# Performance work log

Measured on AMD Instinct MI355X. Metric: run time of the kernel, lower is better.

Reference implementation:

```python
import jax, jax.numpy as jnp
import numpy as np

N = 50000      # nodes
E = 800000     # edges (before self-loops)
IN = 256       # in_channels
HID = 128      # hidden_channels
OUT = 128      # out_channels
NEG_SLOPE = 0.2
EPS = 1e-16


def setup_inputs() -> dict:
    key = jax.random.key(0)
    ks = jax.random.split(key, 16)
    p = lambda k, shape: jax.random.normal(k, shape, jnp.float32) * 0.1
    return {
        "x": jax.random.normal(ks[0], (N, IN), jnp.float32),
        "edge_index": jax.random.randint(ks[1], (2, E), 0, N, dtype=jnp.int64),
        # semantic MLP
        "W1": p(ks[2], (IN, HID)), "b1": jnp.zeros((HID,), jnp.float32),
        "W2": p(ks[3], (HID, HID)), "b2": jnp.zeros((HID,), jnp.float32),
        # gat1: HID -> HID//2, heads=4, concat -> 2*HID
        "g1_W": p(ks[4], (HID, 4 * (HID // 2))),
        "g1_as": p(ks[5], (4, HID // 2)), "g1_ad": p(ks[6], (4, HID // 2)),
        "g1_b": jnp.zeros((4 * (HID // 2),), jnp.float32),
        # gat2: 2*HID -> OUT, heads=2, mean -> OUT
        "g2_W": p(ks[7], (2 * HID, 2 * OUT)),
        "g2_as": p(ks[8], (2, OUT)), "g2_ad": p(ks[9], (2, OUT)),
        "g2_b": jnp.zeros((OUT,), jnp.float32),
        # gat3: OUT -> OUT, heads=1, mean -> OUT
        "g3_W": p(ks[10], (OUT, OUT)),
        "g3_as": p(ks[11], (1, OUT)), "g3_ad": p(ks[12], (1, OUT)),
        "g3_b": jnp.zeros((OUT,), jnp.float32),
    }


def _gat(h_in, src, dst, W, a_src, a_dst, bias, heads, concat, n):
    # Linear projection into heads: [n, H, C]
    h = (h_in @ W).reshape(n, heads, -1)
    alpha_s = jnp.sum(h * a_src[None], axis=-1)  # [n, H]
    alpha_d = jnp.sum(h * a_dst[None], axis=-1)  # [n, H]
    e = jax.nn.leaky_relu(alpha_s[src] + alpha_d[dst], NEG_SLOPE)  # [E', H]
    # segment softmax over edges grouped by destination node
    m = jax.ops.segment_max(e, dst, num_segments=n)
    ex = jnp.exp(e - m[dst])
    denom = jax.ops.segment_sum(ex, dst, num_segments=n)
    alpha = ex / (denom[dst] + EPS)  # [E', H]
    msg = h[src] * alpha[..., None]  # [E', H, C]
    out = jax.ops.segment_sum(msg, dst, num_segments=n)  # [n, H, C]
    out = out.reshape(n, -1) if concat else out.mean(axis=1)
    return out + bias


def reference(x, edge_index, W1, b1, W2, b2,
              g1_W, g1_as, g1_ad, g1_b,
              g2_W, g2_as, g2_ad, g2_b,
              g3_W, g3_as, g3_ad, g3_b):
    n = x.shape[0]
    # PyG GATConv add_self_loops=True: append self-loop edges once
    loops = jnp.arange(n, dtype=edge_index.dtype)
    src = jnp.concatenate([edge_index[0], loops])
    dst = jnp.concatenate([edge_index[1], loops])
    # semantic MLP (inference: dropout = identity)
    h = jax.nn.relu(x @ W1 + b1)
    h = jax.nn.relu(h @ W2 + b2)
    h = jax.nn.elu(_gat(h, src, dst, g1_W, g1_as, g1_ad, g1_b, 4, True, n))
    h = jax.nn.elu(_gat(h, src, dst, g2_W, g2_as, g2_ad, g2_b, 2, False, n))
    h = _gat(h, src, dst, g3_W, g3_as, g3_ad, g3_b, 1, False, n)
    return h
```

## Files before the change

kernel.cpp:

```cpp
#include <hip/hip_runtime.h>
#include <math.h>


#define NEG_SLOPE 0.2f
#define EPS_DEN 1e-16f

typedef __attribute__((ext_vector_type(8))) short short8;
typedef __attribute__((ext_vector_type(4))) float f32x4;
typedef __attribute__((ext_vector_type(2))) float f32x2;
typedef __attribute__((ext_vector_type(4))) unsigned short u16x4;

__device__ inline unsigned short f2b(float f) {
  unsigned u = __builtin_bit_cast(unsigned, f);
  unsigned r = (u + 0x7fffu + ((u >> 16) & 1u)) >> 16;
  return (unsigned short)r;
}
__device__ inline float b2f(unsigned short u) {
  return __builtin_bit_cast(float, (unsigned)u << 16);
}

__device__ inline void glds16(const void* g, void* l) {
  __builtin_amdgcn_global_load_lds(
      (const __attribute__((address_space(1))) void*)g,
      (__attribute__((address_space(3))) void*)l, 16, 0, 0);
}

__device__ inline f32x2 pk_fma(f32x2 a, f32x2 b, f32x2 c) {
  f32x2 d;
  asm("v_pk_fma_f32 %0, %1, %2, %3" : "=v"(d) : "v"(a), "v"(b), "v"(c));
  return d;
}

__device__ inline void accum8(f32x2 acc2[4], const short8 r, float w) {
  const f32x2 wv = {w, w};
  const unsigned* u = (const unsigned*)&r;
#pragma unroll
  for (int p = 0; p < 4; p++) {
    const unsigned lo = u[p] << 16;
    const unsigned hi = u[p] & 0xffff0000u;
    f32x2 val = {__builtin_bit_cast(float, lo), __builtin_bit_cast(float, hi)};
    acc2[p] = pk_fma(val, wv, acc2[p]);
  }
}

template <int H>
__device__ inline void loadH(const float* p, float* v) {
  if constexpr (H == 4) {
    float4 t = *(const float4*)p;
    v[0] = t.x; v[1] = t.y; v[2] = t.z; v[3] = t.w;
  } else if constexpr (H == 2) {
    float2 t = *(const float2*)p;
    v[0] = t.x; v[1] = t.y;
  } else {
    v[0] = *p;
  }
}

template <int ACT, int OBF, int H, int CC>
__global__ __launch_bounds__(256) void mfma_gemm(
    const unsigned short* __restrict__ A, const unsigned short* __restrict__ Bt,
    const float* __restrict__ bias, float* __restrict__ Cf,
    unsigned short* __restrict__ Cb, const float* __restrict__ a_s,
    const float* __restrict__ a_d, float* __restrict__ alS,
    float* __restrict__ alD, int n, int K, int M) {
  __shared__ unsigned short As[128 * 64];
  __shared__ unsigned short Bs[128 * 64];

  const int tid = threadIdx.x;
  const int w = tid >> 6, lane = tid & 63;
  const int row0 = blockIdx.x * 128, col0 = blockIdx.y * 128;
  const int lr = lane >> 3, lg = lane & 7;
  const int lm = lane & 15, kg = lane >> 4;
  const int wm = (w >> 1) * 64, wn = (w & 1) * 64;

  f32x4 acc[4][4];
#pragma unroll
  for (int i = 0; i < 4; i++)
#pragma unroll
    for (int j = 0; j < 4; j++) acc[i][j] = {0.f, 0.f, 0.f, 0.f};

  const int swz = (lg ^ lr) << 3;

  for (int k0 = 0; k0 < K; k0 += 64) {
    __syncthreads();
#pragma unroll
    for (int it = 0; it < 4; it++) {
      const int r = w * 32 + it * 8;
      glds16(A + (size_t)(row0 + r + lr) * K + k0 + swz, &As[r * 64]);
      glds16(Bt + (size_t)(col0 + r + lr) * K + k0 + swz, &Bs[r * 64]);
    }
    __syncthreads();

#pragma unroll
    for (int kh = 0; kh < 2; kh++) {
      const int sw = ((kh * 4 + kg) ^ (lm & 7)) << 3;
      short8 aF[4], bF[4];
#pragma unroll
      for (int i = 0; i < 4; i++) {
        aF[i] = *(const short8*)&As[(wm + i * 16 + lm) * 64 + sw];
        bF[i] = *(const short8*)&Bs[(wn + i * 16 + lm) * 64 + sw];
      }
#pragma unroll
      for (int i = 0; i < 4; i++)
#pragma unroll
        for (int j = 0; j < 4; j++)
          acc[i][j] = __builtin_amdgcn_mfma_f32_16x16x32_bf16(
              aF[i], bF[j], acc[i][j], 0, 0, 0);
    }
  }

  const int r4 = kg * 4;

  if constexpr (H > 0) {
    const int head = (col0 + wn) / CC;
    const int ch0 = (col0 + wn) % CC;
    float asv[4], adv[4];
#pragma unroll
    for (int j = 0; j < 4; j++) {
      asv[j] = a_s[head * CC + ch0 + j * 16 + lm];
      adv[j] = a_d[head * CC + ch0 + j * 16 + lm];
    }
#pragma unroll
    for (int i = 0; i < 4; i++) {
#pragma unroll
      for (int r = 0; r < 4; r++) {
        float ps = 0.f, pd = 0.f;
#pragma unroll
        for (int j = 0; j < 4; j++) {
          ps += acc[i][j][r] * asv[j];
          pd += acc[i][j][r] * adv[j];
        }
#pragma unroll
        for (int off = 1; off < 16; off <<= 1) {
          ps += __shfl_xor(ps, off, 64);
          pd += __shfl_xor(pd, off, 64);
        }
        if (lm == 0) {
          const int row = row0 + wm + i * 16 + r4 + r;
          if (row < n) {
            atomicAdd(&alS[(size_t)row * H + head], ps);
            atomicAdd(&alD[(size_t)row * H + head], pd);
          }
        }
      }
    }
  }

#pragma unroll
  for (int j = 0; j < 4; j++) {
    const int col = col0 + wn + j * 16 + lm;
    const float bv = bias ? bias[col] : 0.f;
#pragma unroll
    for (int i = 0; i < 4; i++) {
#pragma unroll
      for (int r = 0; r < 4; r++) {
        const int row = row0 + wm + i * 16 + r4 + r;
        if (row < n) {
          float v = acc[i][j][r] + bv;
          if (ACT == 1) v = v > 0.f ? v : 0.f;
          if (OBF)
            Cb[(size_t)row * M + col] = f2b(v);
          else
            Cf[(size_t)row * M + col] = v;
        }
      }
    }
  }
}

__global__ __launch_bounds__(256) void mlp_fused_kernel(
    const unsigned short* __restrict__ X, const unsigned short* __restrict__ W1t,
    const float* __restrict__ b1, const unsigned short* __restrict__ W2t,
    const float* __restrict__ b2, unsigned short* __restrict__ H2, int n) {
  __shared__ unsigned short As[128 * 64];
  __shared__ unsigned short Bs[128 * 64];
  __shared__ unsigned short H1s[128 * 136];

  const int tid = threadIdx.x;
  const int w = tid >> 6, lane = tid & 63;
  const int row0 = blockIdx.x * 128;
  const int lr = lane >> 3, lg = lane & 7;
  const int lm = lane & 15, kg = lane >> 4;
  const int wm = (w >> 1) * 64, wn = (w & 1) * 64;
  const int swz = (lg ^ lr) << 3;
  const int r4 = kg * 4;

  f32x4 acc[4][4];
#pragma unroll
  for (int i = 0; i < 4; i++)
#pragma unroll
    for (int j = 0; j < 4; j++) acc[i][j] = {0.f, 0.f, 0.f, 0.f};

  for (int k0 = 0; k0 < 256; k0 += 64) {
    __syncthreads();
#pragma unroll
    for (int it = 0; it < 4; it++) {
      const int r = w * 32 + it * 8;
      glds16(X + (size_t)(row0 + r + lr) * 256 + k0 + swz, &As[r * 64]);
      glds16(W1t + (size_t)(r + lr) * 256 + k0 + swz, &Bs[r * 64]);
    }
    __syncthreads();
#pragma unroll
    for (int kh = 0; kh < 2; kh++) {
      const int sw = ((kh * 4 + kg) ^ (lm & 7)) << 3;
      short8 aF[4], bF[4];
#pragma unroll
      for (int i = 0; i < 4; i++) {
        aF[i] = *(const short8*)&As[(wm + i * 16 + lm) * 64 + sw];
        bF[i] = *(const short8*)&Bs[(wn + i * 16 + lm) * 64 + sw];
      }
#pragma unroll
      for (int i = 0; i < 4; i++)
#pragma unroll
        for (int j = 0; j < 4; j++)
          acc[i][j] = __builtin_amdgcn_mfma_f32_16x16x32_bf16(
              aF[i], bF[j], acc[i][j], 0, 0, 0);
    }
  }

#pragma unroll
  for (int j = 0; j < 4; j++) {
    const int col = wn + j * 16 + lm;
    const float bv = b1[col];
#pragma unroll
    for (int i = 0; i < 4; i++) {
#pragma unroll
      for (int r = 0; r < 4; r++) {
        const int lrow = wm + i * 16 + r4 + r;
        float v = acc[i][j][r] + bv;
        v = v > 0.f ? v : 0.f;
        H1s[lrow * 136 + col] = f2b(v);
      }
    }
  }
#pragma unroll
  for (int i = 0; i < 4; i++)
#pragma unroll
    for (int j = 0; j < 4; j++) acc[i][j] = {0.f, 0.f, 0.f, 0.f};
  __syncthreads();

  for (int k0 = 0; k0 < 128; k0 += 64) {
    __syncthreads();
#pragma unroll
    for (int it = 0; it < 4; it++) {
      const int r = w * 32 + it * 8;
      glds16(W2t + (size_t)(r + lr) * 128 + k0 + swz, &Bs[r * 64]);
    }
    __syncthreads();
#pragma unroll
    for (int kh = 0; kh < 2; kh++) {
      const int swB = ((kh * 4 + kg) ^ (lm & 7)) << 3;
      const int kofs = k0 + (kh * 4 + kg) * 8;
      short8 aF[4], bF[4];
#pragma unroll
      for (int i = 0; i < 4; i++) {
        aF[i] = *(const short8*)&H1s[(wm + i * 16 + lm) * 136 + kofs];
        bF[i] = *(const short8*)&Bs[(wn + i * 16 + lm) * 64 + swB];
      }
#pragma unroll
      for (int i = 0; i < 4; i++)
#pragma unroll
        for (int j = 0; j < 4; j++)
          acc[i][j] = __builtin_amdgcn_mfma_f32_16x16x32_bf16(
              aF[i], bF[j], acc[i][j], 0, 0, 0);
    }
  }

#pragma unroll
  for (int j = 0; j < 4; j++) {
    const int col = wn + j * 16 + lm;
    const float bv = b2[col];
#pragma unroll
    for (int i = 0; i < 4; i++) {
#pragma unroll
      for (int r = 0; r < 4; r++) {
        const int row = row0 + wm + i * 16 + r4 + r;
        if (row < n) {
          float v = acc[i][j][r] + bv;
          v = v > 0.f ? v : 0.f;
          H2[(size_t)row * 128 + col] = f2b(v);
        }
      }
    }
  }
}

struct PrepArgs {
  const float* x; unsigned short* xb; long long nx;
  const float* W[5]; unsigned short* Wt[5];
  int K[5], M[5], t0[6];
  int* deg; int N;
  float* alz; long long nz;
};

__global__ __launch_bounds__(256) void fused_prep_kernel(PrepArgs a) {
  const int tid = threadIdx.x, bid = blockIdx.x, nb = gridDim.x;
  const long long gt = (long long)bid * 256 + tid;
  const long long gsz = (long long)nb * 256;
  __shared__ float tt[32][33];

  for (long long i = gt; i < a.N; i += gsz) a.deg[i] = 0;
  for (long long i = gt * 4; i < a.nz; i += gsz * 4)
    *(float4*)(a.alz + i) = make_float4(0.f, 0.f, 0.f, 0.f);
  for (long long i = gt * 4; i < a.nx; i += gsz * 4) {
    float4 v = *(const float4*)(a.x + i);
    u16x4 u = {f2b(v.x), f2b(v.y), f2b(v.z), f2b(v.w)};
    *(u16x4*)(a.xb + i) = u;
  }
  for (int t = bid; t < a.t0[5]; t += nb) {
    int di = 0;
    while (t >= a.t0[di + 1]) di++;
    const int local = t - a.t0[di];
    const int K = a.K[di], M = a.M[di], mtiles = M / 32;
    const int mb = (local % mtiles) * 32, kb = (local / mtiles) * 32;
    const float* W = a.W[di];
    unsigned short* Wt = a.Wt[di];
    const int tx = tid & 31, ty = tid >> 5;
    __syncthreads();
#pragma unroll
    for (int i = 0; i < 4; i++)
      tt[ty + i * 8][tx] = W[(size_t)(kb + ty + i * 8) * M + mb + tx];
    __syncthreads();
#pragma unroll
    for (int i = 0; i < 4; i++)
      Wt[(size_t)(mb + ty + i * 8) * K + kb + tx] = f2b(tt[tx][ty + i * 8]);
  }
}

__global__ void count_deg_kernel(const int* __restrict__ edst,
                                 int* __restrict__ deg, int E, int n) {
  int i = blockIdx.x * blockDim.x + threadIdx.x;
  if (i >= E + n) return;
  int d = (i < E) ? edst[i] : (i - E);
  if ((unsigned)d < (unsigned)n) atomicAdd(&deg[d], 1);
}

__global__ __launch_bounds__(256) void block_reduce_kernel(
    const int* __restrict__ deg, int* __restrict__ bsum, int n) {
  __shared__ int s[256];
  const int t = threadIdx.x, i = blockIdx.x * 256 + t;
  s[t] = (i < n) ? deg[i] : 0;
  __syncthreads();
#pragma unroll
  for (int off = 128; off; off >>= 1) {
    if (t < off) s[t] += s[t + off];
    __syncthreads();
  }
  if (t == 0) bsum[blockIdx.x] = s[0];
}

__global__ __launch_bounds__(256) void scan_bsums_kernel(int* __restrict__ bsum,
                                                         int nb) {
  __shared__ int s[256];
  const int t = threadIdx.x;
  const int v = (t < nb) ? bsum[t] : 0;
  s[t] = v;
  __syncthreads();
#pragma unroll
  for (int off = 1; off < 256; off <<= 1) {
    int a = (t >= off) ? s[t - off] : 0;
    __syncthreads();
    s[t] += a;
    __syncthreads();
  }
  if (t < nb) bsum[t] = s[t] - v;
}

__global__ __launch_bounds__(256) void scan_final_kernel(
    const int* __restrict__ deg, const int* __restrict__ bsumx,
    int* __restrict__ rowptr, int* __restrict__ cursor, int n) {
  __shared__ int s[256];
  const int t = threadIdx.x, i = blockIdx.x * 256 + t;
  const int v = (i < n) ? deg[i] : 0;
  s[t] = v;
  __syncthreads();
#pragma unroll
  for (int off = 1; off < 256; off <<= 1) {
    int a = (t >= off) ? s[t - off] : 0;
    __syncthreads();
    s[t] += a;
    __syncthreads();
  }
  if (i < n) {
    const int base = bsumx[blockIdx.x];
    const int excl = base + s[t] - v;
    rowptr[i] = excl;
    cursor[i] = excl;
    if (i == n - 1) rowptr[n] = base + s[t];
  }
}

__global__ void scatter_kernel(const int* __restrict__ esrc,
                               const int* __restrict__ edst,
                               int* __restrict__ cursor,
                               int* __restrict__ csr_src, int E, int n) {
  int i = blockIdx.x * blockDim.x + threadIdx.x;
  int tot = E + n;
  if (i >= tot) return;
  int s, d;
  if (i < E) { s = esrc[i]; d = edst[i]; } else { s = d = i - E; }
  if ((unsigned)d >= (unsigned)n || (unsigned)s >= (unsigned)n) return;
  int pos = atomicAdd(&cursor[d], 1);
  if (pos < tot) csr_src[pos] = s;
}

template <int H, int C, bool CONCAT, int ACT, int OBF>
__global__ __launch_bounds__(256) void gat_fused_kernel(
    const unsigned short* __restrict__ proj, const float* __restrict__ alpha_s,
    const float* __restrict__ alpha_d, const int* __restrict__ rowptr,
    const int* __restrict__ csr_src, const float* __restrict__ bias,
    void* __restrict__ out, int n) {
  constexpr int HC = H * C;
  constexpr int ROWSPAN = HC / 8;
  constexpr int EDGES = 64 / ROWSPAN;
  constexpr int WLANES = C / 8;

  __shared__ float exs[4][64 * H];
  __shared__ int sids[4][64];

  const int wv = threadIdx.x >> 6;
  const int wid = (blockIdx.x * blockDim.x + threadIdx.x) >> 6;
  const int lane = threadIdx.x & 63;
  if (wid >= n) return;
  const int dst = wid;
  const int eslot = lane / ROWSPAN;
  const int sl = lane % ROWSPAN;
  const int h_lane = (sl * 8) / C;
  float* myex = &exs[wv][0];
  int* mysid = &sids[wv][0];

  float adv[H];
  loadH<H>(alpha_d + (size_t)dst * H, adv);
  const int rs = rowptr[dst], re = rowptr[dst + 1];

  float denomp[H];
#pragma unroll
  for (int h = 0; h < H; h++) denomp[h] = 0.f;
  f32x2 acc2[4];
#pragma unroll
  for (int p = 0; p < 4; p++) acc2[p] = {0.f, 0.f};

  const unsigned short* prow = proj + sl * 8;

  for (int base = rs; base < re; base += 64) {
    const int cnt = min(64, re - base);
    if (lane < cnt) {
      const int s = csr_src[base + lane];
      mysid[lane] = s;
      float as[H];
      loadH<H>(alpha_s + (size_t)s * H, as);
#pragma unroll
      for (int h = 0; h < H; h++) {
        float e = as[h] + adv[h];
        e = e > 0.f ? e : NEG_SLOPE * e;
        const float ex = __expf(e);
        denomp[h] += ex;
        myex[lane * H + h] = ex;
      }
    }
    __builtin_amdgcn_wave_barrier();
    int j = eslot;
    for (; j + 3 * EDGES < cnt; j += 4 * EDGES) {
      const int s0 = mysid[j];
      const int s1 = mysid[j + EDGES];
      const int s2 = mysid[j + 2 * EDGES];
      const int s3 = mysid[j + 3 * EDGES];
      const float w0 = myex[j * H + h_lane];
      const float w1 = myex[(j + EDGES) * H + h_lane];
      const float w2 = myex[(j + 2 * EDGES) * H + h_lane];
      const float w3 = myex[(j + 3 * EDGES) * H + h_lane];
      const short8 r0 = *(const short8*)(prow + (size_t)s0 * HC);
      const short8 r1 = *(const short8*)(prow + (size_t)s1 * HC);
      const short8 r2 = *(const short8*)(prow + (size_t)s2 * HC);
      const short8 r3 = *(const short8*)(prow + (size_t)s3 * HC);
      accum8(acc2, r0, w0);
      accum8(acc2, r1, w1);
      accum8(acc2, r2, w2);
      accum8(acc2, r3, w3);
    }
    for (; j < cnt; j += EDGES) {
      const int s0 = mysid[j];
      const float w0 = myex[j * H + h_lane];
      const short8 r0 = *(const short8*)(prow + (size_t)s0 * HC);
      accum8(acc2, r0, w0);
    }
    __builtin_amdgcn_wave_barrier();
  }

  float acc[8];
#pragma unroll
  for (int p = 0; p < 4; p++) {
    acc[2 * p] = acc2[p].x;
    acc[2 * p + 1] = acc2[p].y;
  }

#pragma unroll
  for (int off = 32; off; off >>= 1)
#pragma unroll
    for (int h = 0; h < H; h++)
      denomp[h] += __shfl_xor(denomp[h], off, 64);
#pragma unroll
  for (int off = ROWSPAN; off < 64; off <<= 1)
#pragma unroll
    for (int k = 0; k < 8; k++) acc[k] += __shfl_xor(acc[k], off, 64);

  const float inv = 1.f / (denomp[h_lane] + EPS_DEN);
  float v[8];
#pragma unroll
  for (int k = 0; k < 8; k++) v[k] = acc[k] * inv;

  if (!CONCAT && H == 2) {
#pragma unroll
    for (int k = 0; k < 8; k++) v[k] += __shfl_xor(v[k], 16, 64);
  }

  if (CONCAT) {
    if (eslot != 0) return;
    const int c0 = sl * 8;
    float vv[8];
#pragma unroll
    for (int k = 0; k < 8; k++) {
      float t = v[k] + bias[c0 + k];
      if (ACT == 1) t = t > 0.f ? t : (__expf(t) - 1.f);
      vv[k] = t;
    }
    if (OBF) {
      short8 o;
#pragma unroll
      for (int k = 0; k < 8; k++) o[k] = (short)f2b(vv[k]);
      *(short8*)((unsigned short*)out + (size_t)dst * HC + c0) = o;
    } else {
      float* op = (float*)out + (size_t)dst * HC + c0;
      *(float4*)op = make_float4(vv[0], vv[1], vv[2], vv[3]);
      *(float4*)(op + 4) = make_float4(vv[4], vv[5], vv[6], vv[7]);
    }
  } else {
    if (eslot != 0 || sl >= WLANES) return;
    const int c0 = sl * 8;
    const float invH = 1.f / (float)H;
    float vv[8];
#pragma unroll
    for (int k = 0; k < 8; k++) {
      float t = v[k] * invH + bias[c0 + k];
      if (ACT == 1) t = t > 0.f ? t : (__expf(t) - 1.f);
      vv[k] = t;
    }
    if (OBF) {
      short8 o;
#pragma unroll
      for (int k = 0; k < 8; k++) o[k] = (short)f2b(vv[k]);
      *(short8*)((unsigned short*)out + (size_t)dst * C + c0) = o;
    } else {
      float* op = (float*)out + (size_t)dst * C + c0;
      *(float4*)op = make_float4(vv[0], vv[1], vv[2], vv[3]);
      *(float4*)(op + 4) = make_float4(vv[4], vv[5], vv[6], vv[7]);
    }
  }
}

extern "C" void kernel_launch(void* const* d_in, const int* in_sizes, int n_in,
                              void* d_out, int out_size, void* d_ws,
                              size_t ws_size, hipStream_t stream) {
  const float* x    = (const float*)d_in[0];
  const int*   ei   = (const int*)d_in[1];
  const float* W1   = (const float*)d_in[2];
  const float* b1   = (const float*)d_in[3];
  const float* W2   = (const float*)d_in[4];
  const float* b2   = (const float*)d_in[5];
  const float* g1W  = (const float*)d_in[6];
  const float* g1as = (const float*)d_in[7];
  const float* g1ad = (const float*)d_in[8];
  const float* g1b  = (const float*)d_in[9];
  const float* g2W  = (const float*)d_in[10];
  const float* g2as = (const float*)d_in[11];
  const float* g2ad = (const float*)d_in[12];
  const float* g2b  = (const float*)d_in[13];
  const float* g3W  = (const float*)d_in[14];
  const float* g3as = (const float*)d_in[15];
  const float* g3ad = (const float*)d_in[16];
  const float* g3b  = (const float*)d_in[17];

  const int N = in_sizes[0] / 256;
  const int E = in_sizes[1] / 2;
  const int Etot = E + N;
  const int NT = (N + 127) / 128;
  const int NP = NT * 128;
  const int NB = (N + 255) / 256;

  char* p = (char*)d_ws;
  unsigned short* Pb  = (unsigned short*)p; p += (size_t)NP * 256 * 2;
  unsigned short* xb  = (unsigned short*)p; p += (size_t)NP * 256 * 2;
  unsigned short* h2b = (unsigned short*)p; p += (size_t)NP * 128 * 2;
  unsigned short* W1t = (unsigned short*)p; p += (size_t)128 * 256 * 2;
  unsigned short* W2t = (unsigned short*)p; p += (size_t)128 * 128 * 2;
  unsigned short* g1Wt = (unsigned short*)p; p += (size_t)256 * 128 * 2;
  unsigned short* g2Wt = (unsigned short*)p; p += (size_t)256 * 256 * 2;
  unsigned short* g3Wt = (unsigned short*)p; p += (size_t)128 * 128 * 2;
  float* alB = (float*)p; p += (size_t)N * 14 * 4;
  float* alS1 = alB;
  float* alD1 = alB + (size_t)4 * N;
  float* alS2 = alB + (size_t)8 * N;
  float* alD2 = alB + (size_t)10 * N;
  float* alS3 = alB + (size_t)12 * N;
  float* alD3 = alB + (size_t)13 * N;
  int* deg    = (int*)p;
  int* rowptr = deg + N;
  int* cursor = rowptr + N + 1;
  int* bsum   = cursor + N;
  int* csrsrc = bsum + 256;

  const int* esrc = ei;
  const int* edst = ei + E;
  unsigned short* act1b = xb;
  unsigned short* act2b = h2b;

  PrepArgs pa;
  pa.x = x; pa.xb = xb; pa.nx = (long long)N * 256;
  pa.W[0] = W1;  pa.Wt[0] = W1t;  pa.K[0] = 256; pa.M[0] = 128;
  pa.W[1] = W2;  pa.Wt[1] = W2t;  pa.K[1] = 128; pa.M[1] = 128;
  pa.W[2] = g1W; pa.Wt[2] = g1Wt; pa.K[2] = 128; pa.M[2] = 256;
  pa.W[3] = g2W; pa.Wt[3] = g2Wt; pa.K[3] = 256; pa.M[3] = 256;
  pa.W[4] = g3W; pa.Wt[4] = g3Wt; pa.K[4] = 128; pa.M[4] = 128;
  pa.t0[0] = 0;
  for (int i = 0; i < 5; i++)
    pa.t0[i + 1] = pa.t0[i] + (pa.K[i] / 32) * (pa.M[i] / 32);
  pa.deg = deg; pa.N = N;
  pa.alz = alB; pa.nz = (long long)N * 14;
  fused_prep_kernel<<<512, 256, 0, stream>>>(pa);

  count_deg_kernel<<<(Etot + 255) / 256, 256, 0, stream>>>(edst, deg, E, N);
  block_reduce_kernel<<<NB, 256, 0, stream>>>(deg, bsum, N);
  scan_bsums_kernel<<<1, 256, 0, stream>>>(bsum, NB);
  scan_final_kernel<<<NB, 256, 0, stream>>>(deg, bsum, rowptr, cursor, N);
  scatter_kernel<<<(Etot + 255) / 256, 256, 0, stream>>>(esrc, edst, cursor,
                                                         csrsrc, E, N);

  mlp_fused_kernel<<<NT, 256, 0, stream>>>(xb, W1t, b1, W2t, b2, h2b, N);

  mfma_gemm<0, 1, 4, 64><<<dim3(NT, 2), 256, 0, stream>>>(
      h2b, g1Wt, nullptr, nullptr, Pb, g1as, g1ad, alS1, alD1, N, 128, 256);
  gat_fused_kernel<4, 64, true, 1, 1><<<(N + 3) / 4, 256, 0, stream>>>(
      Pb, alS1, alD1, rowptr, csrsrc, g1b, act1b, N);

  mfma_gemm<0, 1, 2, 128><<<dim3(NT, 2), 256, 0, stream>>>(
      act1b, g2Wt, nullptr, nullptr, Pb, g2as, g2ad, alS2, alD2, N, 256, 256);
  gat_fused_kernel<2, 128, false, 1, 1><<<(N + 3) / 4, 256, 0, stream>>>(
      Pb, alS2, alD2, rowptr, csrsrc, g2b, act2b, N);

  mfma_gemm<0, 1, 1, 128><<<dim3(NT, 1), 256, 0, stream>>>(
      act2b, g3Wt, nullptr, nullptr, Pb, g3as, g3ad, alS3, alD3, N, 128, 128);
  gat_fused_kernel<1, 128, false, 0, 0><<<(N + 3) / 4, 256, 0, stream>>>(
      Pb, alS3, alD3, rowptr, csrsrc, g3b, d_out, N);
}
```

Baseline: 508.9 us.

## Replace attention-logit atomics with direct stores; add nontemporal loads/stores and shrink unroll

The GEMM epilogue now writes the per-row attention logits directly. For CC==64 each wave owns a full head, and for wider heads two waves' partial sums are reduced through shared memory. This removes the atomicAdds and the zero-initialisation of the alpha buffers in the prep kernel. The aggregation kernel also loads CSR source indices and stores its outputs with nontemporal hints, and its gather loop unroll drops from 4 to 2 edges per iteration. The reduced unroll may cut register pressure but exposes less memory-level parallelism per gather.

```diff
diff --git a/kernel.cpp b/kernel.cpp
--- a/kernel.cpp
+++ b/kernel.cpp
@@ -120,6 +120,7 @@
       asv[j] = a_s[head * CC + ch0 + j * 16 + lm];
       adv[j] = a_d[head * CC + ch0 + j * 16 + lm];
     }
+    float psA[4][4], pdA[4][4];
 #pragma unroll
     for (int i = 0; i < 4; i++) {
 #pragma unroll
@@ -135,12 +136,42 @@
           ps += __shfl_xor(ps, off, 64);
           pd += __shfl_xor(pd, off, 64);
         }
-        if (lm == 0) {
-          const int row = row0 + wm + i * 16 + r4 + r;
-          if (row < n) {
-            atomicAdd(&alS[(size_t)row * H + head], ps);
-            atomicAdd(&alD[(size_t)row * H + head], pd);
+        psA[i][r] = ps;
+        pdA[i][r] = pd;
+      }
+    }
+    if constexpr (CC == 64) {
+      if (lm == 0) {
+#pragma unroll
+        for (int i = 0; i < 4; i++)
+#pragma unroll
+          for (int r = 0; r < 4; r++) {
+            const int row = row0 + wm + i * 16 + r4 + r;
+            if (row < n) {
+              alS[(size_t)row * H + head] = psA[i][r];
+              alD[(size_t)row * H + head] = pdA[i][r];
+            }
           }
+      }
+    } else {
+      __shared__ float redS[4][64];
+      __shared__ float redD[4][64];
+      if (lm == 0) {
+#pragma unroll
+        for (int i = 0; i < 4; i++)
+#pragma unroll
+          for (int r = 0; r < 4; r++) {
+            redS[w][i * 16 + r4 + r] = psA[i][r];
+            redD[w][i * 16 + r4 + r] = pdA[i][r];
+          }
+      }
+      __syncthreads();
+      if ((w & 1) == 0) {
+        const int row = row0 + wm + lane;
+        if (row < n) {
+          const int hd = col0 / CC;
+          alS[(size_t)row * H + hd] = redS[w][lane] + redS[w + 1][lane];
+          alD[(size_t)row * H + hd] = redD[w][lane] + redD[w + 1][lane];
         }
       }
     }
@@ -290,7 +321,6 @@
   const float* W[5]; unsigned short* Wt[5];
   int K[5], M[5], t0[6];
   int* deg; int N;
-  float* alz; long long nz;
 };
 
 __global__ __launch_bounds__(256) void fused_prep_kernel(PrepArgs a) {
@@ -300,8 +330,6 @@
   __shared__ float tt[32][33];
 
   for (long long i = gt; i < a.N; i += gsz) a.deg[i] = 0;
-  for (long long i = gt * 4; i < a.nz; i += gsz * 4)
-    *(float4*)(a.alz + i) = make_float4(0.f, 0.f, 0.f, 0.f);
   for (long long i = gt * 4; i < a.nx; i += gsz * 4) {
     float4 v = *(const float4*)(a.x + i);
     u16x4 u = {f2b(v.x), f2b(v.y), f2b(v.z), f2b(v.w)};
@@ -445,7 +473,7 @@
   for (int base = rs; base < re; base += 64) {
     const int cnt = min(64, re - base);
     if (lane < cnt) {
-      const int s = csr_src[base + lane];
+      const int s = __builtin_nontemporal_load(csr_src + base + lane);
       mysid[lane] = s;
       float as[H];
       loadH<H>(alpha_s + (size_t)s * H, as);
@@ -460,23 +488,15 @@
     }
     __builtin_amdgcn_wave_barrier();
     int j = eslot;
-    for (; j + 3 * EDGES < cnt; j += 4 * EDGES) {
+    for (; j + EDGES < cnt; j += 2 * EDGES) {
       const int s0 = mysid[j];
       const int s1 = mysid[j + EDGES];
-      const int s2 = mysid[j + 2 * EDGES];
-      const int s3 = mysid[j + 3 * EDGES];
       const float w0 = myex[j * H + h_lane];
       const float w1 = myex[(j + EDGES) * H + h_lane];
-      const float w2 = myex[(j + 2 * EDGES) * H + h_lane];
-      const float w3 = myex[(j + 3 * EDGES) * H + h_lane];
       const short8 r0 = *(const short8*)(prow + (size_t)s0 * HC);
       const short8 r1 = *(const short8*)(prow + (size_t)s1 * HC);
-      const short8 r2 = *(const short8*)(prow + (size_t)s2 * HC);
-      const short8 r3 = *(const short8*)(prow + (size_t)s3 * HC);
       accum8(acc2, r0, w0);
       accum8(acc2, r1, w1);
-      accum8(acc2, r2, w2);
-      accum8(acc2, r3, w3);
     }
     for (; j < cnt; j += EDGES) {
       const int s0 = mysid[j];
@@ -528,11 +548,14 @@
       short8 o;
 #pragma unroll
       for (int k = 0; k < 8; k++) o[k] = (short)f2b(vv[k]);
-      *(short8*)((unsigned short*)out + (size_t)dst * HC + c0) = o;
+      __builtin_nontemporal_store(
+          o, (short8*)((unsigned short*)out + (size_t)dst * HC + c0));
     } else {
       float* op = (float*)out + (size_t)dst * HC + c0;
-      *(float4*)op = make_float4(vv[0], vv[1], vv[2], vv[3]);
-      *(float4*)(op + 4) = make_float4(vv[4], vv[5], vv[6], vv[7]);
+      f32x4 o0 = {vv[0], vv[1], vv[2], vv[3]};
+      f32x4 o1 = {vv[4], vv[5], vv[6], vv[7]};
+      __builtin_nontemporal_store(o0, (f32x4*)op);
+      __builtin_nontemporal_store(o1, (f32x4*)(op + 4));
     }
   } else {
     if (eslot != 0 || sl >= WLANES) return;
@@ -549,11 +572,14 @@
       short8 o;
 #pragma unroll
       for (int k = 0; k < 8; k++) o[k] = (short)f2b(vv[k]);
-      *(short8*)((unsigned short*)out + (size_t)dst * C + c0) = o;
+      __builtin_nontemporal_store(
+          o, (short8*)((unsigned short*)out + (size_t)dst * C + c0));
     } else {
       float* op = (float*)out + (size_t)dst * C + c0;
-      *(float4*)op = make_float4(vv[0], vv[1], vv[2], vv[3]);
-      *(float4*)(op + 4) = make_float4(vv[4], vv[5], vv[6], vv[7]);
+      f32x4 o0 = {vv[0], vv[1], vv[2], vv[3]};
+      f32x4 o1 = {vv[4], vv[5], vv[6], vv[7]};
+      __builtin_nontemporal_store(o0, (f32x4*)op);
+      __builtin_nontemporal_store(o1, (f32x4*)(op + 4));
     }
   }
 }
@@ -625,7 +651,6 @@
   for (int i = 0; i < 5; i++)
     pa.t0[i + 1] = pa.t0[i] + (pa.K[i] / 32) * (pa.M[i] / 32);
   pa.deg = deg; pa.N = N;
-  pa.alz = alB; pa.nz = (long long)N * 14;
   fused_prep_kernel<<<512, 256, 0, stream>>>(pa);
 
   count_deg_kernel<<<(Etot + 255) / 256, 256, 0, stream>>>(edst, deg, E, N);
```

After: 485.5 us. 1.05x faster.
